# Optimization experiments

Hardware: AMD Instinct MI355X
Metric: run time of the kernel (lower is better)

The kernel has to match this reference:

```python
import jax, jax.numpy as jnp
import numpy as np

N = 50000        # nodes
E = 1_600_000    # edges (avg degree 32)
G = 512          # graphs
F_IN = 9         # node features
H = 64           # hidden dim
ED = 1           # edge feature dim


def _lin(k, fo, fi):
    w = jax.random.normal(k, (fo, fi), jnp.float32) * (1.0 / np.sqrt(fi))
    b = jnp.zeros((fo,), jnp.float32)
    return w, b


def setup_inputs() -> dict:
    key = jax.random.key(0)
    ks = jax.random.split(key, 16)
    x = jax.random.normal(ks[0], (N, F_IN), jnp.float32)
    edge_index = jax.random.randint(ks[1], (2, E), 0, N, dtype=jnp.int64)
    edge_attr = jax.random.normal(ks[2], (E, ED), jnp.float32)
    batch = jnp.sort(jax.random.randint(ks[3], (N,), 0, G, dtype=jnp.int64))
    B_total = jax.random.uniform(ks[4], (G,), jnp.float32) * 100.0
    terminal_mask = jax.random.randint(ks[5], (N,), 0, 2, dtype=jnp.int32)
    c_cost = jax.random.uniform(ks[6], (N,), jnp.float32)
    # conv1: edge lin (ED->F_IN), nn = Linear(F_IN,H), Linear(H,H)
    e1_w, e1_b = _lin(ks[7], F_IN, ED)
    w1a, b1a = _lin(ks[8], H, F_IN)
    w1b, b1b = _lin(ks[9], H, H)
    # conv2: edge lin (ED->H), nn = Linear(H,H), Linear(H,H)
    e2_w, e2_b = _lin(ks[10], H, ED)
    w2a, b2a = _lin(ks[11], H, H)
    w2b, b2b = _lin(ks[12], H, H)
    # readout: Linear(H,H//2), Linear(H//2,1)
    wr1, br1 = _lin(ks[13], H // 2, H)
    wr2, br2 = _lin(ks[14], 1, H // 2)
    return dict(x=x, edge_index=edge_index, edge_attr=edge_attr, batch=batch,
                B_total=B_total, terminal_mask=terminal_mask, c_cost=c_cost,
                e1_w=e1_w, e1_b=e1_b, w1a=w1a, b1a=b1a, w1b=w1b, b1b=b1b,
                e2_w=e2_w, e2_b=e2_b, w2a=w2a, b2a=b2a, w2b=w2b, b2b=b2b,
                wr1=wr1, br1=br1, wr2=wr2, br2=br2)


def _gine(x, src, dst, edge_attr, ew, eb, wa, ba, wb, bb):
    # GINEConv (eps=0): nn(x + sum_j relu(x_j + W_e e_ji))
    e = edge_attr @ ew.T + eb                    # [E, F]
    m = jax.nn.relu(x[src] + e)                  # [E, F] gather + edge fuse
    aggr = jax.ops.segment_sum(m, dst, num_segments=N)  # scatter-add -> [N, F]
    h = x + aggr
    h = jax.nn.relu(h @ wa.T + ba)
    h = jax.nn.relu(h @ wb.T + bb)
    return h


def reference(x, edge_index, edge_attr, batch, B_total, terminal_mask, c_cost,
              e1_w, e1_b, w1a, b1a, w1b, b1b,
              e2_w, e2_b, w2a, b2a, w2b, b2b,
              wr1, br1, wr2, br2):
    src, dst = edge_index[0], edge_index[1]
    h = _gine(x, src, dst, edge_attr, e1_w, e1_b, w1a, b1a, w1b, b1b)
    h = _gine(h, src, dst, edge_attr, e2_w, e2_b, w2a, b2a, w2b, b2b)
    pi_raw = jax.nn.sigmoid((jax.nn.relu(h @ wr1.T + br1) @ wr2.T + br2))[:, 0]
    pi_raw = pi_raw * (1.0 - terminal_mask.astype(jnp.float32))
    node_expenses = pi_raw * c_cost
    total_expenses = jax.ops.segment_sum(node_expenses, batch, num_segments=G)
    ratio = jnp.minimum(B_total[batch] / (total_expenses[batch] + 1e-12), 1.0)
    return pi_raw * ratio
```

## Files before the change

kernel.cpp:

```cpp
#include <hip/hip_runtime.h>
#include <hip/hip_fp16.h>
#include <math.h>

#define N_NODES 50000
#define N_EDGES 1600000
#define N_GRAPHS 512
#define F_IN 9
#define H 64
#define N_BUCKETS ((N_NODES + 255) >> 8)
#define EPB 4096
#define N_SBLK ((N_EDGES + EPB - 1) / EPB)
#define FINE_CAP 10240

typedef _Float16 f16x8 __attribute__((ext_vector_type(8)));
typedef float f32x4 __attribute__((ext_vector_type(4)));

__device__ __forceinline__ void pack_weights_body(
        const float* __restrict__ w1a, const float* __restrict__ w1b,
        const float* __restrict__ w2a, const float* __restrict__ w2b,
        const float* __restrict__ wr1,
        __half* __restrict__ pk1Ah, __half* __restrict__ pk1Al,
        __half* __restrict__ pk1Bh, __half* __restrict__ pk1Bl,
        __half* __restrict__ pkAh, __half* __restrict__ pkAl,
        __half* __restrict__ pkBh, __half* __restrict__ pkBl,
        __half* __restrict__ pkRh, __half* __restrict__ pkRl) {
    int t = threadIdx.x;
    for (int i = t; i < 2048; i += 256) {
        int j = i & 7, l = (i >> 3) & 63, tt = i >> 9;
        int q = l >> 4, n = l & 15;
        int k = q * 8 + j;
        float v = (k < F_IN) ? w1a[(tt * 16 + n) * F_IN + k] : 0.f;
        __half h = __float2half(v);
        pk1Ah[i] = h; pk1Al[i] = __float2half(v - __half2float(h));
    }
    for (int i = t; i < 4096; i += 256) {
        int j = i & 7, l = (i >> 3) & 63, c = (i >> 9) & 1, tt = i >> 10;
        int q = l >> 4, n = l & 15;
        int src = (tt * 16 + n) * H + c * 32 + q * 8 + j;
        float v1 = w1b[src], wa = w2a[src], wb = w2b[src];
        __half h1 = __float2half(v1), ah = __float2half(wa), bh = __float2half(wb);
        pk1Bh[i] = h1; pk1Bl[i] = __float2half(v1 - __half2float(h1));
        pkAh[i] = ah; pkAl[i] = __float2half(wa - __half2float(ah));
        pkBh[i] = bh; pkBl[i] = __float2half(wb - __half2float(bh));
    }
    for (int i = t; i < 2048; i += 256) {
        int j = i & 7, l = (i >> 3) & 63, c = (i >> 9) & 1, tt = i >> 10;
        int q = l >> 4, n = l & 15;
        float wr = wr1[(tt * 16 + n) * H + c * 32 + q * 8 + j];
        __half rh = __float2half(wr);
        pkRh[i] = rh; pkRl[i] = __float2half(wr - __half2float(rh));
    }
}

__global__ void bucket_scatter(const int* __restrict__ ei,
                               const float* __restrict__ ea,
                               int* __restrict__ bnext,
                               uint2* __restrict__ ebuk,
                               const float* __restrict__ w1a,
                               const float* __restrict__ w1b,
                               const float* __restrict__ w2a,
                               const float* __restrict__ w2b,
                               const float* __restrict__ wr1,
                               __half* pk1Ah, __half* pk1Al,
                               __half* pk1Bh, __half* pk1Bl,
                               __half* pkAh, __half* pkAl,
                               __half* pkBh, __half* pkBl,
                               __half* pkRh, __half* pkRl) {
    if (blockIdx.x == 0) {
        pack_weights_body(w1a, w1b, w2a, w2b, wr1, pk1Ah, pk1Al, pk1Bh, pk1Bl,
                          pkAh, pkAl, pkBh, pkBl, pkRh, pkRl);
        return;
    }
    __shared__ int cnt[N_BUCKETS];
    __shared__ int gbase[N_BUCKETS];
    for (int i = threadIdx.x; i < N_BUCKETS; i += 256) cnt[i] = 0;
    __syncthreads();
    int base = (blockIdx.x - 1) * EPB;
    int rk[16];
#pragma unroll
    for (int j = 0; j < 16; ++j) {
        int e = base + j * 256 + threadIdx.x;
        rk[j] = -1;
        if (e < N_EDGES) {
            int d = ei[N_EDGES + e];
            int b = d >> 8;
            int r = atomicAdd(&cnt[b], 1);
            rk[j] = (b << 21) | ((d & 255) << 13) | r;
        }
    }
    __syncthreads();
    for (int i = threadIdx.x; i < N_BUCKETS; i += 256)
        gbase[i] = cnt[i] ? atomicAdd(&bnext[i], cnt[i]) : 0;
    __syncthreads();
#pragma unroll
    for (int j = 0; j < 16; ++j) {
        if (rk[j] < 0) continue;
        int e = base + j * 256 + threadIdx.x;
        int b = rk[j] >> 21, dl = (rk[j] >> 13) & 255, r = rk[j] & 8191;
        int slot = gbase[b] + r;
        if (slot >= FINE_CAP) continue;
        unsigned pay = ((unsigned)ei[e] << 16) |
                       (unsigned)__half_as_ushort(__float2half(ea[e]));
        ebuk[(size_t)b * FINE_CAP + slot] = make_uint2(pay, (unsigned)dl);
    }
}

__global__ void __launch_bounds__(256)
bucket_fine(const uint2* __restrict__ ebuk,
            const int* __restrict__ bnext,
            unsigned* __restrict__ ep4,
            int* __restrict__ starts, int* __restrict__ deg) {
    __shared__ unsigned sorted[FINE_CAP];
    __shared__ int cntN[256], offN[256], nxtN[256];
    __shared__ int wsum[4];
    int b = blockIdx.x;
    int base = b * FINE_CAP;
    int count = bnext[b];
    if (count > FINE_CAP) count = FINE_CAP;
    int tid = threadIdx.x;
    cntN[tid] = 0;
    __syncthreads();
    for (int i = tid; i < count; i += 256)
        atomicAdd(&cntN[ebuk[base + i].y], 1);
    __syncthreads();
    int lane = tid & 63, wid = tid >> 6;
    int v = cntN[tid], incl = v;
#pragma unroll
    for (int off = 1; off < 64; off <<= 1) {
        int t = __shfl_up(incl, off, 64);
        if (lane >= off) incl += t;
    }
    if (lane == 63) wsum[wid] = incl;
    __syncthreads();
    int woff = 0;
    for (int w = 0; w < wid; ++w) woff += wsum[w];
    int excl = woff + incl - v;
    offN[tid] = excl;
    nxtN[tid] = 0;
    int n = (b << 8) + tid;
    if (n < N_NODES) { starts[n] = base + excl; deg[n] = v; }
    __syncthreads();
    for (int i = tid; i < count; i += 256) {
        uint2 e = ebuk[base + i];
        int r = atomicAdd(&nxtN[e.y], 1);
        sorted[offN[e.y] + r] = e.x;
    }
    __syncthreads();
    for (int i = tid; i < count; i += 256)
        ep4[base + i] = sorted[i];
}

#define UNPACK_ATTR(P) __half2float(__ushort_as_half((unsigned short)((P) & 0xffffu)))

__global__ void agg1_kernel(const float* __restrict__ x,
                            const int* __restrict__ starts,
                            const int* __restrict__ deg,
                            const unsigned* __restrict__ ep4,
                            const float* __restrict__ e1w,
                            const float* __restrict__ e1b,
                            float* __restrict__ xs) {
    int n = blockIdx.x * (blockDim.x >> 6) + (threadIdx.x >> 6);
    int lane = threadIdx.x & 63;
    if (n >= N_NODES) return;
    int slot = lane >> 4;
    int f = lane & 15;
    int s0 = starts[n], dg = deg[n];
    bool act = f < F_IN;
    float wf = act ? e1w[f] : 0.f;
    float bf = act ? e1b[f] : 0.f;
    float acc = 0.f;
    int j = slot;
    for (; j + 12 < dg; j += 16) {
        unsigned pa = ep4[s0 + j];
        unsigned pb = ep4[s0 + j + 4];
        unsigned pc = ep4[s0 + j + 8];
        unsigned pd = ep4[s0 + j + 12];
        float xa_ = act ? x[(pa >> 16) * F_IN + f] : 0.f;
        float xb_ = act ? x[(pb >> 16) * F_IN + f] : 0.f;
        float xc_ = act ? x[(pc >> 16) * F_IN + f] : 0.f;
        float xd_ = act ? x[(pd >> 16) * F_IN + f] : 0.f;
        if (act) {
            acc += fmaxf(xa_ + UNPACK_ATTR(pa) * wf + bf, 0.f)
                 + fmaxf(xb_ + UNPACK_ATTR(pb) * wf + bf, 0.f)
                 + fmaxf(xc_ + UNPACK_ATTR(pc) * wf + bf, 0.f)
                 + fmaxf(xd_ + UNPACK_ATTR(pd) * wf + bf, 0.f);
        }
    }
    for (; j < dg; j += 4) {
        unsigned p = ep4[s0 + j];
        float xv = act ? x[(p >> 16) * F_IN + f] : 0.f;
        float m = xv + UNPACK_ATTR(p) * wf + bf;
        acc += act ? fmaxf(m, 0.f) : 0.f;
    }
    acc += __shfl_xor(acc, 16, 64);
    acc += __shfl_xor(acc, 32, 64);
    if (lane < 32)
        xs[n * 32 + lane] = (lane < F_IN) ? x[n * F_IN + lane] + acc : 0.f;
}

__device__ __forceinline__ void split8(const float* __restrict__ v,
                                       f16x8& hi, f16x8& lo) {
#pragma unroll
    for (int j = 0; j < 8; ++j) {
        _Float16 h = (_Float16)v[j];
        hi[j] = h;
        lo[j] = (_Float16)(v[j] - (float)h);
    }
}

#define TILE3(C, A0H, A0L, A1H, A1L, PH, PL, T) do {                          \
        f16x8 b0h = *(const f16x8*)((PH) + (((T) * 2 + 0) * 64 + lane) * 8);  \
        f16x8 b0l = *(const f16x8*)((PL) + (((T) * 2 + 0) * 64 + lane) * 8);  \
        f16x8 b1h = *(const f16x8*)((PH) + (((T) * 2 + 1) * 64 + lane) * 8);  \
        f16x8 b1l = *(const f16x8*)((PL) + (((T) * 2 + 1) * 64 + lane) * 8);  \
        C = __builtin_amdgcn_mfma_f32_16x16x32_f16(A0H, b0h, C, 0, 0, 0);     \
        C = __builtin_amdgcn_mfma_f32_16x16x32_f16(A0L, b0h, C, 0, 0, 0);     \
        C = __builtin_amdgcn_mfma_f32_16x16x32_f16(A0H, b0l, C, 0, 0, 0);     \
        C = __builtin_amdgcn_mfma_f32_16x16x32_f16(A1H, b1h, C, 0, 0, 0);     \
        C = __builtin_amdgcn_mfma_f32_16x16x32_f16(A1L, b1h, C, 0, 0, 0);     \
        C = __builtin_amdgcn_mfma_f32_16x16x32_f16(A1H, b1l, C, 0, 0, 0);     \
    } while (0)

__global__ void node1_kernel(const float* __restrict__ xs,
                             const __half* __restrict__ pk1Ah, const __half* __restrict__ pk1Al,
                             const float* __restrict__ b1a,
                             const __half* __restrict__ pk1Bh, const __half* __restrict__ pk1Bl,
                             const float* __restrict__ b1b,
                             __half* __restrict__ h1) {
    __shared__ float hbuf[4][16][68];
    int wv = threadIdx.x >> 6;
    int lane = threadIdx.x & 63;
    int gwave = blockIdx.x * 4 + wv;
    bool active = gwave < (N_NODES / 16);
    int base = active ? gwave * 16 : 0;
    int m = lane & 15, q = lane >> 4;
    const _Float16* pAh = (const _Float16*)pk1Ah;
    const _Float16* pAl = (const _Float16*)pk1Al;
    const _Float16* pBh = (const _Float16*)pk1Bh;
    const _Float16* pBl = (const _Float16*)pk1Bl;

    f16x8 ah, al;
    split8(xs + (size_t)(base + m) * 32 + q * 8, ah, al);
#pragma unroll
    for (int t = 0; t < 4; ++t) {
        f32x4 c = {0.f, 0.f, 0.f, 0.f};
        f16x8 bh = *(const f16x8*)(pAh + (t * 64 + lane) * 8);
        f16x8 bl = *(const f16x8*)(pAl + (t * 64 + lane) * 8);
        c = __builtin_amdgcn_mfma_f32_16x16x32_f16(ah, bh, c, 0, 0, 0);
        c = __builtin_amdgcn_mfma_f32_16x16x32_f16(al, bh, c, 0, 0, 0);
        c = __builtin_amdgcn_mfma_f32_16x16x32_f16(ah, bl, c, 0, 0, 0);
        float bias = b1a[t * 16 + m];
#pragma unroll
        for (int r = 0; r < 4; ++r)
            hbuf[wv][q * 4 + r][t * 16 + m] = fmaxf(c[r] + bias, 0.f);
    }
    __syncthreads();
    f16x8 a0h, a0l, a1h, a1l;
    split8(&hbuf[wv][m][q * 8], a0h, a0l);
    split8(&hbuf[wv][m][32 + q * 8], a1h, a1l);
    float tmp[4][4];
#pragma unroll
    for (int t = 0; t < 4; ++t) {
        f32x4 c = {0.f, 0.f, 0.f, 0.f};
        TILE3(c, a0h, a0l, a1h, a1l, pBh, pBl, t);
        float bias = b1b[t * 16 + m];
#pragma unroll
        for (int r = 0; r < 4; ++r)
            tmp[t][r] = fmaxf(c[r] + bias, 0.f);
    }
    __syncthreads();
#pragma unroll
    for (int t = 0; t < 4; ++t)
#pragma unroll
        for (int r = 0; r < 4; ++r)
            hbuf[wv][q * 4 + r][t * 16 + m] = tmp[t][r];
    __syncthreads();
    if (active) {
        int nn = lane >> 2, part = lane & 3;
        f16x8 vlo, vhi;
        const float* rlo = &hbuf[wv][nn][part * 8];
        const float* rhi = &hbuf[wv][nn][32 + part * 8];
#pragma unroll
        for (int j = 0; j < 8; ++j) {
            vlo[j] = (_Float16)rlo[j];
            vhi[j] = (_Float16)rhi[j];
        }
        *(f16x8*)(h1 + (size_t)(base + nn) * 64 + part * 8) = vlo;
        *(f16x8*)(h1 + (size_t)(base + nn) * 64 + 32 + part * 8) = vhi;
    }
}

__global__ void aggphase2_kernel(const __half* __restrict__ h1,
                                 const int* __restrict__ starts,
                                 const int* __restrict__ deg,
                                 const unsigned* __restrict__ ep4,
                                 const float* __restrict__ ew,
                                 const float* __restrict__ eb,
                                 float* __restrict__ htot) {
    int n = blockIdx.x * (blockDim.x >> 6) + (threadIdx.x >> 6);
    int lane = threadIdx.x & 63;
    if (n >= N_NODES) return;
    int s0 = starts[n], dg = deg[n];
    const unsigned* ep = ep4 + s0;
    float wf = ew[lane], bf = eb[lane];
    float acc = 0.f;
#define EDGE1(P, V) acc += fmaxf((V) + UNPACK_ATTR(P) * wf + bf, 0.f)
    int j = 0;
    for (; j + 8 <= dg; j += 8) {
        unsigned p0 = ep[j + 0], p1 = ep[j + 1], p2 = ep[j + 2], p3 = ep[j + 3];
        unsigned p4 = ep[j + 4], p5 = ep[j + 5], p6 = ep[j + 6], p7 = ep[j + 7];
        float v0 = __half2float(h1[(size_t)(p0 >> 16) * 64 + lane]);
        float v1 = __half2float(h1[(size_t)(p1 >> 16) * 64 + lane]);
        float v2 = __half2float(h1[(size_t)(p2 >> 16) * 64 + lane]);
        float v3 = __half2float(h1[(size_t)(p3 >> 16) * 64 + lane]);
        float v4 = __half2float(h1[(size_t)(p4 >> 16) * 64 + lane]);
        float v5 = __half2float(h1[(size_t)(p5 >> 16) * 64 + lane]);
        float v6 = __half2float(h1[(size_t)(p6 >> 16) * 64 + lane]);
        float v7 = __half2float(h1[(size_t)(p7 >> 16) * 64 + lane]);
        EDGE1(p0, v0); EDGE1(p1, v1); EDGE1(p2, v2); EDGE1(p3, v3);
        EDGE1(p4, v4); EDGE1(p5, v5); EDGE1(p6, v6); EDGE1(p7, v7);
    }
    if (j + 4 <= dg) {
        unsigned p0 = ep[j + 0], p1 = ep[j + 1], p2 = ep[j + 2], p3 = ep[j + 3];
        float v0 = __half2float(h1[(size_t)(p0 >> 16) * 64 + lane]);
        float v1 = __half2float(h1[(size_t)(p1 >> 16) * 64 + lane]);
        float v2 = __half2float(h1[(size_t)(p2 >> 16) * 64 + lane]);
        float v3 = __half2float(h1[(size_t)(p3 >> 16) * 64 + lane]);
        EDGE1(p0, v0); EDGE1(p1, v1); EDGE1(p2, v2); EDGE1(p3, v3);
        j += 4;
    }
    for (; j < dg; ++j) {
        unsigned p = ep[j];
        float v = __half2float(h1[(size_t)(p >> 16) * 64 + lane]);
        EDGE1(p, v);
    }
#undef EDGE1
    float self = __half2float(h1[(size_t)n * 64 + lane]);
    htot[(size_t)n * 64 + lane] = self + acc;
}

__global__ void node2_kernel(const float* __restrict__ htot,
                             const __half* __restrict__ pkAh, const __half* __restrict__ pkAl,
                             const float* __restrict__ b2a,
                             const __half* __restrict__ pkBh, const __half* __restrict__ pkBl,
                             const float* __restrict__ b2b,
                             const __half* __restrict__ pkRh, const __half* __restrict__ pkRl,
                             const float* __restrict__ br1,
                             const float* __restrict__ wr2,
                             const float* __restrict__ br2,
                             const int* __restrict__ term,
                             const int* __restrict__ batch,
                             const float* __restrict__ ccost,
                             float* __restrict__ pi,
                             float* __restrict__ te) {
    __shared__ float hbuf[4][16][68];
    int wv = threadIdx.x >> 6;
    int lane = threadIdx.x & 63;
    int gwave = blockIdx.x * 4 + wv;
    bool active = gwave < (N_NODES / 16);
    int base = active ? gwave * 16 : 0;
    int m = lane & 15, q = lane >> 4;
    const _Float16* pAh = (const _Float16*)pkAh;
    const _Float16* pAl = (const _Float16*)pkAl;
    const _Float16* pBh = (const _Float16*)pkBh;
    const _Float16* pBl = (const _Float16*)pkBl;
    const _Float16* pRh = (const _Float16*)pkRh;
    const _Float16* pRl = (const _Float16*)pkRl;

    f16x8 a0h, a0l, a1h, a1l;
    {
        const float* hrow = htot + (size_t)(base + m) * 64;
        split8(hrow + q * 8, a0h, a0l);
        split8(hrow + 32 + q * 8, a1h, a1l);
    }
#pragma unroll
    for (int t = 0; t < 4; ++t) {
        f32x4 c = {0.f, 0.f, 0.f, 0.f};
        TILE3(c, a0h, a0l, a1h, a1l, pAh, pAl, t);
        float bias = b2a[t * 16 + m];
#pragma unroll
        for (int r = 0; r < 4; ++r)
            hbuf[wv][q * 4 + r][t * 16 + m] = fmaxf(c[r] + bias, 0.f);
    }
    __syncthreads();
    split8(&hbuf[wv][m][q * 8], a0h, a0l);
    split8(&hbuf[wv][m][32 + q * 8], a1h, a1l);
    float tmp[4][4];
#pragma unroll
    for (int t = 0; t < 4; ++t) {
        f32x4 c = {0.f, 0.f, 0.f, 0.f};
        TILE3(c, a0h, a0l, a1h, a1l, pBh, pBl, t);
        float bias = b2b[t * 16 + m];
#pragma unroll
        for (int r = 0; r < 4; ++r)
            tmp[t][r] = fmaxf(c[r] + bias, 0.f);
    }
    __syncthreads();
#pragma unroll
    for (int t = 0; t < 4; ++t)
#pragma unroll
        for (int r = 0; r < 4; ++r)
            hbuf[wv][q * 4 + r][t * 16 + m] = tmp[t][r];
    __syncthreads();
    split8(&hbuf[wv][m][q * 8], a0h, a0l);
    split8(&hbuf[wv][m][32 + q * 8], a1h, a1l);
    float partial[4] = {0.f, 0.f, 0.f, 0.f};
#pragma unroll
    for (int t = 0; t < 2; ++t) {
        f32x4 c = {0.f, 0.f, 0.f, 0.f};
        TILE3(c, a0h, a0l, a1h, a1l, pRh, pRl, t);
        float bias = br1[t * 16 + m];
        float wv2 = wr2[t * 16 + m];
#pragma unroll
        for (int r = 0; r < 4; ++r)
            partial[r] += fmaxf(c[r] + bias, 0.f) * wv2;
    }
#pragma unroll
    for (int off = 1; off < 16; off <<= 1) {
        partial[0] += __shfl_xor(partial[0], off, 64);
        partial[1] += __shfl_xor(partial[1], off, 64);
        partial[2] += __shfl_xor(partial[2], off, 64);
        partial[3] += __shfl_xor(partial[3], off, 64);
    }
    if (active && m == 0) {
#pragma unroll
        for (int r = 0; r < 4; ++r) {
            int n = base + q * 4 + r;
            float z = partial[r] + br2[0];
            float sig = 1.f / (1.f + expf(-z));
            float pv = sig * (1.f - (float)term[n]);
            pi[n] = pv;
            float contrib = pv * ccost[n];
            if (contrib != 0.f) atomicAdd(&te[batch[n]], contrib);
        }
    }
}

__global__ void final_kernel(const float* __restrict__ pi,
                             const int* __restrict__ batch,
                             const float* __restrict__ Btot,
                             const float* __restrict__ te,
                             float* __restrict__ out) {
    int n = blockIdx.x * blockDim.x + threadIdx.x;
    if (n >= N_NODES) return;
    int b = batch[n];
    float ratio = fminf(Btot[b] / (te[b] + 1e-12f), 1.f);
    out[n] = pi[n] * ratio;
}

extern "C" void kernel_launch(void* const* d_in, const int* in_sizes, int n_in,
                              void* d_out, int out_size, void* d_ws, size_t ws_size,
                              hipStream_t stream) {
    const float* x     = (const float*)d_in[0];
    const int*   ei    = (const int*)d_in[1];
    const float* ea    = (const float*)d_in[2];
    const int*   batch = (const int*)d_in[3];
    const float* Btot  = (const float*)d_in[4];
    const int*   term  = (const int*)d_in[5];
    const float* ccost = (const float*)d_in[6];
    const float* e1w   = (const float*)d_in[7];
    const float* e1b   = (const float*)d_in[8];
    const float* w1a   = (const float*)d_in[9];
    const float* b1a   = (const float*)d_in[10];
    const float* w1b   = (const float*)d_in[11];
    const float* b1b   = (const float*)d_in[12];
    const float* e2w   = (const float*)d_in[13];
    const float* e2b   = (const float*)d_in[14];
    const float* w2a   = (const float*)d_in[15];
    const float* b2a   = (const float*)d_in[16];
    const float* w2b   = (const float*)d_in[17];
    const float* b2b   = (const float*)d_in[18];
    const float* wr1   = (const float*)d_in[19];
    const float* br1   = (const float*)d_in[20];
    const float* wr2   = (const float*)d_in[21];
    const float* br2   = (const float*)d_in[22];

    char* p = (char*)d_ws;
    int*      bnext  = (int*)p;      p += sizeof(int)      * 256;
    float*    te     = (float*)p;    p += sizeof(float)    * N_GRAPHS;
    int*      starts = (int*)p;      p += sizeof(int)      * N_NODES;
    int*      deg    = (int*)p;      p += sizeof(int)      * N_NODES;
    p = (char*)(((size_t)p + 15) & ~(size_t)15);
    uint2*    ebuk   = (uint2*)p;    p += sizeof(uint2)    * (size_t)N_BUCKETS * FINE_CAP;
    unsigned* ep4    = (unsigned*)p; p += sizeof(unsigned) * (size_t)N_BUCKETS * FINE_CAP;
    __half*   h1     = (__half*)p;   p += sizeof(__half)   * (size_t)N_NODES * 64;
    float*    htot   = (float*)p;    p += sizeof(float)    * (size_t)N_NODES * 64;
    float*    xs     = (float*)p;    p += sizeof(float)    * (size_t)N_NODES * 32;
    float*    pi     = (float*)p;    p += sizeof(float)    * N_NODES;
    __half*   pk1Ah  = (__half*)p;   p += sizeof(__half)   * 2048;
    __half*   pk1Al  = (__half*)p;   p += sizeof(__half)   * 2048;
    __half*   pk1Bh  = (__half*)p;   p += sizeof(__half)   * 4096;
    __half*   pk1Bl  = (__half*)p;   p += sizeof(__half)   * 4096;
    __half*   pkAh   = (__half*)p;   p += sizeof(__half)   * 4096;
    __half*   pkAl   = (__half*)p;   p += sizeof(__half)   * 4096;
    __half*   pkBh   = (__half*)p;   p += sizeof(__half)   * 4096;
    __half*   pkBl   = (__half*)p;   p += sizeof(__half)   * 4096;
    __half*   pkRh   = (__half*)p;   p += sizeof(__half)   * 2048;
    __half*   pkRl   = (__half*)p;   p += sizeof(__half)   * 2048;
    float*    out    = (float*)d_out;

    hipMemsetAsync(d_ws, 0, sizeof(int) * 256 + sizeof(float) * N_GRAPHS, stream);

    bucket_scatter<<<1 + N_SBLK, 256, 0, stream>>>(ei, ea, bnext, ebuk,
                                                   w1a, w1b, w2a, w2b, wr1,
                                                   pk1Ah, pk1Al, pk1Bh, pk1Bl,
                                                   pkAh, pkAl, pkBh, pkBl, pkRh, pkRl);
    bucket_fine<<<N_BUCKETS, 256, 0, stream>>>(ebuk, bnext, ep4, starts, deg);
    agg1_kernel<<<(N_NODES + 3) / 4, 256, 0, stream>>>(x, starts, deg, ep4, e1w, e1b, xs);
    node1_kernel<<<(N_NODES / 16 + 3) / 4, 256, 0, stream>>>(xs, pk1Ah, pk1Al, b1a,
                                                             pk1Bh, pk1Bl, b1b, h1);
    aggphase2_kernel<<<(N_NODES + 3) / 4, 256, 0, stream>>>(h1, starts, deg, ep4,
                                                            e2w, e2b, htot);
    node2_kernel<<<(N_NODES / 16 + 3) / 4, 256, 0, stream>>>(htot,
                                                             pkAh, pkAl, b2a,
                                                             pkBh, pkBl, b2b,
                                                             pkRh, pkRl, br1,
                                                             wr2, br2, term,
                                                             batch, ccost, pi, te);
    final_kernel<<<(N_NODES + 255) / 256, 256, 0, stream>>>(pi, batch, Btot, te, out);
}
```

Measured before the change: 254.2 us.

## Replace two-level bucket sort with global atomic counting sort for CSR build

```diff
diff --git a/kernel.cpp b/kernel.cpp
--- a/kernel.cpp
+++ b/kernel.cpp
@@ -8,9 +8,8 @@
 #define F_IN 9
 #define H 64
 #define N_BUCKETS ((N_NODES + 255) >> 8)
-#define EPB 4096
-#define N_SBLK ((N_EDGES + EPB - 1) / EPB)
 #define FINE_CAP 10240
+#define EP4_TOTAL ((size_t)N_BUCKETS * FINE_CAP)
 
 typedef _Float16 f16x8 __attribute__((ext_vector_type(8)));
 typedef float f32x4 __attribute__((ext_vector_type(4)));
@@ -52,79 +51,43 @@
     }
 }
 
-__global__ void bucket_scatter(const int* __restrict__ ei,
-                               const float* __restrict__ ea,
-                               int* __restrict__ bnext,
-                               uint2* __restrict__ ebuk,
-                               const float* __restrict__ w1a,
-                               const float* __restrict__ w1b,
-                               const float* __restrict__ w2a,
-                               const float* __restrict__ w2b,
-                               const float* __restrict__ wr1,
-                               __half* pk1Ah, __half* pk1Al,
-                               __half* pk1Bh, __half* pk1Bl,
-                               __half* pkAh, __half* pkAl,
-                               __half* pkBh, __half* pkBl,
-                               __half* pkRh, __half* pkRl) {
+__global__ void count_kernel(const int* __restrict__ ei,
+                             int* __restrict__ deg,
+                             const float* __restrict__ w1a,
+                             const float* __restrict__ w1b,
+                             const float* __restrict__ w2a,
+                             const float* __restrict__ w2b,
+                             const float* __restrict__ wr1,
+                             __half* pk1Ah, __half* pk1Al,
+                             __half* pk1Bh, __half* pk1Bl,
+                             __half* pkAh, __half* pkAl,
+                             __half* pkBh, __half* pkBl,
+                             __half* pkRh, __half* pkRl) {
     if (blockIdx.x == 0) {
         pack_weights_body(w1a, w1b, w2a, w2b, wr1, pk1Ah, pk1Al, pk1Bh, pk1Bl,
                           pkAh, pkAl, pkBh, pkBl, pkRh, pkRl);
         return;
     }
-    __shared__ int cnt[N_BUCKETS];
-    __shared__ int gbase[N_BUCKETS];
-    for (int i = threadIdx.x; i < N_BUCKETS; i += 256) cnt[i] = 0;
-    __syncthreads();
-    int base = (blockIdx.x - 1) * EPB;
-    int rk[16];
-#pragma unroll
-    for (int j = 0; j < 16; ++j) {
+    int base = (blockIdx.x - 1) * 2048;
+#pragma unroll
+    for (int j = 0; j < 8; ++j) {
         int e = base + j * 256 + threadIdx.x;
-        rk[j] = -1;
         if (e < N_EDGES) {
             int d = ei[N_EDGES + e];
-            int b = d >> 8;
-            int r = atomicAdd(&cnt[b], 1);
-            rk[j] = (b << 21) | ((d & 255) << 13) | r;
+            atomicAdd(&deg[d], 1);
         }
     }
-    __syncthreads();
-    for (int i = threadIdx.x; i < N_BUCKETS; i += 256)
-        gbase[i] = cnt[i] ? atomicAdd(&bnext[i], cnt[i]) : 0;
-    __syncthreads();
-#pragma unroll
-    for (int j = 0; j < 16; ++j) {
-        if (rk[j] < 0) continue;
-        int e = base + j * 256 + threadIdx.x;
-        int b = rk[j] >> 21, dl = (rk[j] >> 13) & 255, r = rk[j] & 8191;
-        int slot = gbase[b] + r;
-        if (slot >= FINE_CAP) continue;
-        unsigned pay = ((unsigned)ei[e] << 16) |
-                       (unsigned)__half_as_ushort(__float2half(ea[e]));
-        ebuk[(size_t)b * FINE_CAP + slot] = make_uint2(pay, (unsigned)dl);
-    }
-}
-
-__global__ void __launch_bounds__(256)
-bucket_fine(const uint2* __restrict__ ebuk,
-            const int* __restrict__ bnext,
-            unsigned* __restrict__ ep4,
-            int* __restrict__ starts, int* __restrict__ deg) {
-    __shared__ unsigned sorted[FINE_CAP];
-    __shared__ int cntN[256], offN[256], nxtN[256];
+}
+
+__global__ void scan_init_kernel(const int* __restrict__ deg,
+                                 int* __restrict__ starts,
+                                 int* __restrict__ cur) {
     __shared__ int wsum[4];
-    int b = blockIdx.x;
-    int base = b * FINE_CAP;
-    int count = bnext[b];
-    if (count > FINE_CAP) count = FINE_CAP;
-    int tid = threadIdx.x;
-    cntN[tid] = 0;
-    __syncthreads();
-    for (int i = tid; i < count; i += 256)
-        atomicAdd(&cntN[ebuk[base + i].y], 1);
-    __syncthreads();
+    int b = blockIdx.x, tid = threadIdx.x;
+    int n = (b << 8) + tid;
+    int v = (n < N_NODES) ? deg[n] : 0;
     int lane = tid & 63, wid = tid >> 6;
-    int v = cntN[tid], incl = v;
+    int incl = v;
 #pragma unroll
     for (int off = 1; off < 64; off <<= 1) {
         int t = __shfl_up(incl, off, 64);
@@ -135,19 +98,33 @@
     int woff = 0;
     for (int w = 0; w < wid; ++w) woff += wsum[w];
     int excl = woff + incl - v;
-    offN[tid] = excl;
-    nxtN[tid] = 0;
-    int n = (b << 8) + tid;
-    if (n < N_NODES) { starts[n] = base + excl; deg[n] = v; }
-    __syncthreads();
-    for (int i = tid; i < count; i += 256) {
-        uint2 e = ebuk[base + i];
-        int r = atomicAdd(&nxtN[e.y], 1);
-        sorted[offN[e.y] + r] = e.x;
-    }
-    __syncthreads();
-    for (int i = tid; i < count; i += 256)
-        ep4[base + i] = sorted[i];
+    if (n < N_NODES) {
+        int s = b * FINE_CAP + excl;
+        starts[n] = s;
+        cur[n] = s;
+    }
+}
+
+__global__ void place_kernel(const int* __restrict__ ei,
+                             const float* __restrict__ ea,
+                             int* __restrict__ cur,
+                             unsigned* __restrict__ ep4) {
+    int base = blockIdx.x * 2048;
+#pragma unroll
+    for (int j = 0; j < 8; ++j) {
+        int e = base + j * 256 + threadIdx.x;
+        if (e < N_EDGES) {
+            int d = ei[N_EDGES + e];
+            int s = ei[e];
+            float a = ea[e];
+            int slot = atomicAdd(&cur[d], 1);
+            if (slot < (int)EP4_TOTAL) {
+                unsigned pay = ((unsigned)s << 16) |
+                               (unsigned)__half_as_ushort(__float2half(a));
+                ep4[slot] = pay;
+            }
+        }
+    }
 }
 
 #define UNPACK_ATTR(P) __half2float(__ushort_as_half((unsigned short)((P) & 0xffffu)))
@@ -476,13 +453,12 @@
     const float* br2   = (const float*)d_in[22];
 
     char* p = (char*)d_ws;
-    int*      bnext  = (int*)p;      p += sizeof(int)      * 256;
     float*    te     = (float*)p;    p += sizeof(float)    * N_GRAPHS;
+    int*      deg    = (int*)p;      p += sizeof(int)      * N_NODES;
     int*      starts = (int*)p;      p += sizeof(int)      * N_NODES;
-    int*      deg    = (int*)p;      p += sizeof(int)      * N_NODES;
+    int*      cur    = (int*)p;      p += sizeof(int)      * N_NODES;
     p = (char*)(((size_t)p + 15) & ~(size_t)15);
-    uint2*    ebuk   = (uint2*)p;    p += sizeof(uint2)    * (size_t)N_BUCKETS * FINE_CAP;
-    unsigned* ep4    = (unsigned*)p; p += sizeof(unsigned) * (size_t)N_BUCKETS * FINE_CAP;
+    unsigned* ep4    = (unsigned*)p; p += sizeof(unsigned) * EP4_TOTAL;
     __half*   h1     = (__half*)p;   p += sizeof(__half)   * (size_t)N_NODES * 64;
     float*    htot   = (float*)p;    p += sizeof(float)    * (size_t)N_NODES * 64;
     float*    xs     = (float*)p;    p += sizeof(float)    * (size_t)N_NODES * 32;
@@ -499,13 +475,15 @@
     __half*   pkRl   = (__half*)p;   p += sizeof(__half)   * 2048;
     float*    out    = (float*)d_out;
 
-    hipMemsetAsync(d_ws, 0, sizeof(int) * 256 + sizeof(float) * N_GRAPHS, stream);
-
-    bucket_scatter<<<1 + N_SBLK, 256, 0, stream>>>(ei, ea, bnext, ebuk,
-                                                   w1a, w1b, w2a, w2b, wr1,
-                                                   pk1Ah, pk1Al, pk1Bh, pk1Bl,
-                                                   pkAh, pkAl, pkBh, pkBl, pkRh, pkRl);
-    bucket_fine<<<N_BUCKETS, 256, 0, stream>>>(ebuk, bnext, ep4, starts, deg);
+    hipMemsetAsync(d_ws, 0, sizeof(float) * N_GRAPHS + sizeof(int) * N_NODES, stream);
+
+    const int EDGE_BLOCKS = (N_EDGES + 2047) / 2048;
+    count_kernel<<<1 + EDGE_BLOCKS, 256, 0, stream>>>(ei, deg,
+                                                      w1a, w1b, w2a, w2b, wr1,
+                                                      pk1Ah, pk1Al, pk1Bh, pk1Bl,
+                                                      pkAh, pkAl, pkBh, pkBl, pkRh, pkRl);
+    scan_init_kernel<<<N_BUCKETS, 256, 0, stream>>>(deg, starts, cur);
+    place_kernel<<<EDGE_BLOCKS, 256, 0, stream>>>(ei, ea, cur, ep4);
     agg1_kernel<<<(N_NODES + 3) / 4, 256, 0, stream>>>(x, starts, deg, ep4, e1w, e1b, xs);
     node1_kernel<<<(N_NODES / 16 + 3) / 4, 256, 0, stream>>>(xs, pk1Ah, pk1Al, b1a,
                                                              pk1Bh, pk1Bl, b1b, h1);
```

Result: slower. 404.1 us (+59.0%).
